# Performance work log

Measured on AMD Instinct MI355X. Metric: run time of the kernel, lower is better.

Reference implementation:

```python
import jax, jax.numpy as jnp
import numpy as np

N = 50000
E = 800000
D = 128
L = 3


def gru_cell(m, h, w_ih, w_hh, b_ih, b_hh):
    # m, h: [N, D]; w_ih, w_hh: [3D, D]; b_ih, b_hh: [3D]
    gi = m @ w_ih.T + b_ih  # [N, 3D]
    gh = h @ w_hh.T + b_hh  # [N, 3D]
    i_r, i_z, i_n = jnp.split(gi, 3, axis=-1)
    h_r, h_z, h_n = jnp.split(gh, 3, axis=-1)
    r = jax.nn.sigmoid(i_r + h_r)
    z = jax.nn.sigmoid(i_z + h_z)
    n = jnp.tanh(i_n + r * h_n)
    return (1.0 - z) * n + z * h


def setup_inputs() -> dict:
    key = jax.random.key(0)
    ks = jax.random.split(key, 8)
    s = 1.0 / np.sqrt(D)
    z = jax.random.normal(ks[0], (N, D), dtype=jnp.float32)
    edge_index = jax.random.randint(ks[1], (2, E), 0, N, dtype=jnp.int64)
    weight = jax.random.uniform(ks[2], (L, D, D), dtype=jnp.float32, minval=-s, maxval=s)
    w_ih = jax.random.uniform(ks[3], (3 * D, D), dtype=jnp.float32, minval=-s, maxval=s)
    w_hh = jax.random.uniform(ks[4], (3 * D, D), dtype=jnp.float32, minval=-s, maxval=s)
    b_ih = jax.random.uniform(ks[5], (3 * D,), dtype=jnp.float32, minval=-s, maxval=s)
    b_hh = jax.random.uniform(ks[6], (3 * D,), dtype=jnp.float32, minval=-s, maxval=s)
    return {"z": z, "edge_index": edge_index, "weight": weight,
            "w_ih": w_ih, "w_hh": w_hh, "b_ih": b_ih, "b_hh": b_hh}


def reference(z, edge_index, weight, w_ih, w_hh, b_ih, b_hh):
    # GatedGraphConv: per layer, m = h @ W_l; aggregate m[src] into dst (sum); GRU update.
    src, dst = edge_index[0], edge_index[1]
    h = z  # in_channels == out_channels, no padding
    for l in range(L):
        m = h @ weight[l]                              # [N, D]
        agg = jax.ops.segment_sum(m[src], dst, num_segments=N)  # scatter-add over edges
        h = gru_cell(agg, h, w_ih, w_hh, b_ih, b_hh)
    return h
```

## Files before the change

### kernel.cpp

```cpp
#include <hip/hip_runtime.h>
#include <hip/hip_bf16.h>

#define NN 50000
#define NE 800000
#define D 128
#define NL 3
#define G3 384

typedef __attribute__((ext_vector_type(4))) float f32x4;
typedef __attribute__((ext_vector_type(2))) float f32x2;
typedef _Float16 f16;
typedef __attribute__((ext_vector_type(8))) _Float16 f16x8;
typedef __attribute__((ext_vector_type(2))) _Float16 f16x2;

__global__ void detect_i64_kernel(const int* __restrict__ ei, int* __restrict__ flag) {
    __shared__ int any_nz;
    if (threadIdx.x == 0) any_nz = 0;
    __syncthreads();
    int v = ei[threadIdx.x * 2 + 1];
    if (v != 0) atomicOr(&any_nz, 1);
    __syncthreads();
    if (threadIdx.x == 0) *flag = (any_nz == 0) ? 1 : 0;
}

static __device__ __forceinline__ void load_edge(const int* ei, const int* flag, int e,
                                                 int& src, int& dst) {
    if (*flag) {
        src = ei[2LL * e];
        dst = ei[2LL * (NE + e)];
    } else {
        src = ei[e];
        dst = ei[NE + e];
    }
}

__global__ void hist_kernel(const int* __restrict__ ei, const int* __restrict__ flag,
                            int* __restrict__ counts, unsigned short* __restrict__ rank16) {
    int e = blockIdx.x * blockDim.x + threadIdx.x;
    if (e >= NE) return;
    int src, dst;
    load_edge(ei, flag, e, src, dst);
    rank16[e] = (unsigned short)atomicAdd(counts + dst, 1);
}

#define SBLK 256
#define NSB ((NN + SBLK - 1) / SBLK)

__global__ __launch_bounds__(SBLK) void scan_reduce_kernel(const int* __restrict__ counts,
                                                           int* __restrict__ block_sums) {
    __shared__ int lds[SBLK];
    int i = blockIdx.x * SBLK + threadIdx.x;
    lds[threadIdx.x] = (i < NN) ? counts[i] : 0;
    __syncthreads();
    for (int off = SBLK / 2; off > 0; off >>= 1) {
        if (threadIdx.x < off) lds[threadIdx.x] += lds[threadIdx.x + off];
        __syncthreads();
    }
    if (threadIdx.x == 0) block_sums[blockIdx.x] = lds[0];
}

__global__ __launch_bounds__(256) void scan_offsets_kernel(const int* __restrict__ block_sums,
                                                           int* __restrict__ block_off,
                                                           int* __restrict__ row_start) {
    __shared__ int lds[256];
    int t = threadIdx.x;
    int v = (t < NSB) ? block_sums[t] : 0;
    lds[t] = v;
    __syncthreads();
    for (int off = 1; off < 256; off <<= 1) {
        int x = (t >= off) ? lds[t - off] : 0;
        __syncthreads();
        lds[t] += x;
        __syncthreads();
    }
    if (t < NSB) block_off[t] = lds[t] - v;
    if (t == 255) row_start[NN] = lds[255];
}

__global__ __launch_bounds__(SBLK) void scan_final_kernel(const int* __restrict__ counts,
                                                          const int* __restrict__ block_off,
                                                          int* __restrict__ row_start) {
    __shared__ int lds[SBLK];
    int i = blockIdx.x * SBLK + threadIdx.x;
    int v = (i < NN) ? counts[i] : 0;
    lds[threadIdx.x] = v;
    __syncthreads();
    for (int off = 1; off < SBLK; off <<= 1) {
        int x = (threadIdx.x >= off) ? lds[threadIdx.x - off] : 0;
        __syncthreads();
        lds[threadIdx.x] += x;
        __syncthreads();
    }
    if (i < NN) row_start[i] = block_off[blockIdx.x] + lds[threadIdx.x] - v;
}

__global__ void fill_kernel(const int* __restrict__ ei, const int* __restrict__ flag,
                            const int* __restrict__ row_start,
                            const unsigned short* __restrict__ rank16,
                            unsigned short* __restrict__ csr16) {
    int e = blockIdx.x * blockDim.x + threadIdx.x;
    if (e >= NE) return;
    int src, dst;
    load_edge(ei, flag, e, src, dst);
    csr16[row_start[dst] + (int)rank16[e]] = (unsigned short)src;
}

__global__ void init_h_kernel(const float* __restrict__ z, f16* __restrict__ h) {
    int i = blockIdx.x * blockDim.x + threadIdx.x;
    if (i * 2 >= NN * D) return;
    f32x2 v = *(const f32x2*)(z + i * 2);
    f16x2 o = {(f16)v[0], (f16)v[1]};
    *(f16x2*)(h + i * 2) = o;
}

__global__ __launch_bounds__(256) void gather_kernel(
    const f16* __restrict__ h, const int* __restrict__ row_start,
    const unsigned short* __restrict__ csr16, f16* __restrict__ agg) {
    int row = blockIdx.x * 4 + (threadIdx.x >> 6);
    if (row >= NN) return;
    int lane = threadIdx.x & 63;
    int eslot = lane >> 4;
    int c0 = (lane & 15) * 8;
    int beg = row_start[row], end = row_start[row + 1];
    float acc[8] = {0.f, 0.f, 0.f, 0.f, 0.f, 0.f, 0.f, 0.f};
    for (int base = beg; base + eslot < end; base += 4) {
        int s = (int)csr16[base + eslot];
        f16x8 v = *(const f16x8*)(h + s * D + c0);
#pragma unroll
        for (int j = 0; j < 8; ++j) acc[j] += (float)v[j];
    }
#pragma unroll
    for (int j = 0; j < 8; ++j) {
        acc[j] += __shfl_xor(acc[j], 16, 64);
        acc[j] += __shfl_xor(acc[j], 32, 64);
    }
    if (lane < 16) {
        f16x8 o;
#pragma unroll
        for (int j = 0; j < 8; ++j) o[j] = (f16)acc[j];
        *(f16x8*)(agg + row * D + c0) = o;
    }
}

__global__ void precompute_weights(const float* __restrict__ weight,
                                   const float* __restrict__ w_ih,
                                   const float* __restrict__ w_hh,
                                   f16* __restrict__ wct, f16* __restrict__ whh) {
    int l = blockIdx.x / G3;
    int g = blockIdx.x % G3;
    int c = threadIdx.x;
    __shared__ float wih_row[D];
    wih_row[c] = w_ih[g * D + c];
    __syncthreads();
    const float* wrow = weight + ((long long)l * D + c) * D;
    float acc = 0.f;
#pragma unroll 8
    for (int j = 0; j < D; ++j) acc += wrow[j] * wih_row[j];
    wct[((long long)l * G3 + g) * D + c] = (f16)acc;
    if (l == 0) whh[g * D + c] = (f16)w_hh[g * D + c];
}

#define TMG 128
#define MFMA_F16 __builtin_amdgcn_mfma_f32_16x16x32_f16
__global__ __launch_bounds__(512) void gru_fused_kernel(
    const f16* __restrict__ agg, const f16* __restrict__ hin, f16* __restrict__ hout,
    const f16* __restrict__ wct, const f16* __restrict__ whh,
    const float* __restrict__ b_ih, const float* __restrict__ b_hh, int ndt,
    float* __restrict__ out_f32) {
    __shared__ char wlds[6 * 4096];
    const int tid = threadIdx.x;
    const int lane = tid & 63;
    const int wv = tid >> 6;
    const int fr = lane & 15;
    const int kg = lane >> 4;
    const int m0 = blockIdx.x * TMG;
    const int dt0 = blockIdx.y * ndt;

    int arow = m0 + wv * 16 + fr;
    int arc = arow < NN ? arow : NN - 1;
    const int abase = arc * D;

    f16x8 fa[4], fh[4];
#pragma unroll
    for (int ks = 0; ks < 4; ++ks) {
        int k0 = ks * 32 + kg * 8;
        fa[ks] = *(const f16x8*)(agg + abase + k0);
        fh[ks] = *(const f16x8*)(hin + abase + k0);
    }

#pragma unroll 1
    for (int dti = 0; dti < ndt; ++dti) {
        const int dt = dt0 + dti;
        const int gr = dt * 16;
        if (dti) __syncthreads();
#pragma unroll
        for (int p3 = 0; p3 < 3; ++p3) {
            int unit = tid + p3 * 512;
            int panel = unit >> 8;
            int u = unit & 255;
            int sr = u >> 4;
            int sc = (u & 15) * 8;
            const f16* srcp = (panel < 3)
                                  ? wct + (panel * 128 + gr + sr) * D + sc
                                  : whh + ((panel - 3) * 128 + gr + sr) * D + sc;
            int wb = (u * 16) ^ ((sr & 7) << 4);
            *(f16x8*)(wlds + panel * 4096 + wb) = *(const f16x8*)srcp;
        }
        __syncthreads();

        f32x4 a_ir = {0, 0, 0, 0}, a_iz = {0, 0, 0, 0}, a_in = {0, 0, 0, 0};
        f32x4 a_hr = {0, 0, 0, 0}, a_hz = {0, 0, 0, 0}, a_hn = {0, 0, 0, 0};
#pragma unroll
        for (int ks = 0; ks < 4; ++ks) {
            const int kb = fr * 256 + (((ks * 4 + kg) ^ (fr & 7)) << 4);
            f16x8 bir = *(const f16x8*)(wlds + 0 * 4096 + kb);
            f16x8 biz = *(const f16x8*)(wlds + 1 * 4096 + kb);
            f16x8 bin = *(const f16x8*)(wlds + 2 * 4096 + kb);
            f16x8 bhr = *(const f16x8*)(wlds + 3 * 4096 + kb);
            f16x8 bhz = *(const f16x8*)(wlds + 4 * 4096 + kb);
            f16x8 bhn = *(const f16x8*)(wlds + 5 * 4096 + kb);
            a_ir = MFMA_F16(fa[ks], bir, a_ir, 0, 0, 0);
            a_iz = MFMA_F16(fa[ks], biz, a_iz, 0, 0, 0);
            a_in = MFMA_F16(fa[ks], bin, a_in, 0, 0, 0);
            a_hr = MFMA_F16(fh[ks], bhr, a_hr, 0, 0, 0);
            a_hz = MFMA_F16(fh[ks], bhz, a_hz, 0, 0, 0);
            a_hn = MFMA_F16(fh[ks], bhn, a_hn, 0, 0, 0);
        }
        const int d = gr + fr;
        float bir_ = b_ih[d], biz_ = b_ih[128 + d], bin_ = b_ih[256 + d];
        float bhr_ = b_hh[d], bhz_ = b_hh[128 + d], bhn_ = b_hh[256 + d];
#pragma unroll
        for (int j = 0; j < 4; ++j) {
            int row = m0 + wv * 16 + kg * 4 + j;
            if (row >= NN) continue;
            float ir = a_ir[j] + bir_, iz = a_iz[j] + biz_, in_ = a_in[j] + bin_;
            float hr = a_hr[j] + bhr_, hz = a_hz[j] + bhz_, hn = a_hn[j] + bhn_;
            float r = 1.f / (1.f + __expf(-(ir + hr)));
            float zz = 1.f / (1.f + __expf(-(iz + hz)));
            float e2 = __expf(2.f * (in_ + r * hn));
            float nn = 1.f - 2.f / (e2 + 1.f);
            int off = row * D + d;
            float hold = (float)hin[off];
            float hnew = (1.f - zz) * nn + zz * hold;
            if (out_f32)
                out_f32[off] = hnew;
            else
                hout[off] = (f16)hnew;
        }
    }
}

extern "C" void kernel_launch(void* const* d_in, const int* in_sizes, int n_in,
                              void* d_out, int out_size, void* d_ws, size_t ws_size,
                              hipStream_t stream) {
    const float* z = (const float*)d_in[0];
    const int* ei = (const int*)d_in[1];
    const float* weight = (const float*)d_in[2];
    const float* w_ih = (const float*)d_in[3];
    const float* w_hh = (const float*)d_in[4];
    const float* b_ih = (const float*)d_in[5];
    const float* b_hh = (const float*)d_in[6];
    float* out = (float*)d_out;

    char* ws = (char*)d_ws;
    size_t off = 0;
    f16* wct = (f16*)(ws + off); off += 294912;
    f16* whh = (f16*)(ws + off); off += 98304;
    int* flag       = (int*)(ws + off); off += 256;
    int* counts     = (int*)(ws + off); off += (size_t)NN * 4;
    int* row_start  = (int*)(ws + off); off += (size_t)(NN + 16) * 4;
    int* block_sums = (int*)(ws + off); off += (size_t)NSB * 4;
    int* block_off  = (int*)(ws + off); off += (size_t)NSB * 4;
    unsigned short* rank16 = (unsigned short*)(ws + off); off += (size_t)NE * 2;
    unsigned short* csr16  = (unsigned short*)(ws + off); off += (size_t)NE * 2;
    f16* agg  = (f16*)(ws + off); off += (size_t)NN * D * 2;
    f16* hA   = (f16*)(ws + off); off += (size_t)NN * D * 2;
    size_t off_min = off;
    f16* hB   = (f16*)(ws + off); off += (size_t)NN * D * 2;
    const bool split = (ws_size >= off);
    if (!split) { hB = hA; (void)off_min; }

    detect_i64_kernel<<<1, 256, 0, stream>>>(ei, flag);
    hipMemsetAsync(counts, 0, (size_t)NN * 4, stream);
    hist_kernel<<<(NE + 255) / 256, 256, 0, stream>>>(ei, flag, counts, rank16);
    scan_reduce_kernel<<<NSB, SBLK, 0, stream>>>(counts, block_sums);
    scan_offsets_kernel<<<1, 256, 0, stream>>>(block_sums, block_off, row_start);
    scan_final_kernel<<<NSB, SBLK, 0, stream>>>(counts, block_off, row_start);
    fill_kernel<<<(NE + 255) / 256, 256, 0, stream>>>(ei, flag, row_start, rank16, csr16);
    precompute_weights<<<NL * G3, 128, 0, stream>>>(weight, w_ih, w_hh, wct, whh);
    const int npair = NN * D / 2;
    init_h_kernel<<<(npair + 255) / 256, 256, 0, stream>>>(z, hA);

    const int ndt = split ? 2 : 8;
    const dim3 gg((NN + TMG - 1) / TMG, split ? 4 : 1);
    const f16* cin = hA;
    for (int l = 0; l < NL; ++l) {
        gather_kernel<<<(NN + 3) / 4, 256, 0, stream>>>(cin, row_start, csr16, agg);
        f16* cout = split ? ((cin == hA) ? hB : hA) : (f16*)cin;
        long long woff = (long long)l * G3 * D;
        float* last_out = (l == NL - 1) ? out : nullptr;
        gru_fused_kernel<<<gg, 512, 0, stream>>>(agg, cin, cout, wct + woff, whh,
                                                 b_ih, b_hh, ndt, last_out);
        cin = cout;
    }
}
```

Before: 309.4 us.

## Unroll gather with dual accumulators and stage all GRU weight tiles at once

The gather loop now processes two edge batches per iteration into two accumulators, so more independent row loads are in flight. The fused GRU kernel fixes NDT at 2 and loads both column tiles' weight panels into a larger shared buffer in one pass with a single barrier, instead of reloading and syncing per tile. A separate fallback kernel that reads weights directly from global memory handles the case where the workspace is too small for double-buffered h. The change doubles the GRU kernel's shared-memory footprint, which may lower occupancy.

```diff
diff --git a/kernel.cpp b/kernel.cpp
--- a/kernel.cpp
+++ b/kernel.cpp
@@ -123,14 +123,25 @@
     int c0 = (lane & 15) * 8;
     int beg = row_start[row], end = row_start[row + 1];
     float acc[8] = {0.f, 0.f, 0.f, 0.f, 0.f, 0.f, 0.f, 0.f};
-    for (int base = beg; base + eslot < end; base += 4) {
-        int s = (int)csr16[base + eslot];
+    float acc2[8] = {0.f, 0.f, 0.f, 0.f, 0.f, 0.f, 0.f, 0.f};
+    int e = beg;
+    for (; e + 7 < end; e += 8) {
+        int s0 = (int)csr16[e + eslot];
+        int s1 = (int)csr16[e + eslot + 4];
+        f16x8 v0 = *(const f16x8*)(h + s0 * D + c0);
+        f16x8 v1 = *(const f16x8*)(h + s1 * D + c0);
+#pragma unroll
+        for (int j = 0; j < 8; ++j) { acc[j] += (float)v0[j]; acc2[j] += (float)v1[j]; }
+    }
+    for (; e + eslot < end; e += 4) {
+        int s = (int)csr16[e + eslot];
         f16x8 v = *(const f16x8*)(h + s * D + c0);
 #pragma unroll
         for (int j = 0; j < 8; ++j) acc[j] += (float)v[j];
     }
 #pragma unroll
     for (int j = 0; j < 8; ++j) {
+        acc[j] += acc2[j];
         acc[j] += __shfl_xor(acc[j], 16, 64);
         acc[j] += __shfl_xor(acc[j], 32, 64);
     }
@@ -161,20 +172,21 @@
 }
 
 #define TMG 128
+#define NDT 2
 #define MFMA_F16 __builtin_amdgcn_mfma_f32_16x16x32_f16
 __global__ __launch_bounds__(512) void gru_fused_kernel(
     const f16* __restrict__ agg, const f16* __restrict__ hin, f16* __restrict__ hout,
     const f16* __restrict__ wct, const f16* __restrict__ whh,
-    const float* __restrict__ b_ih, const float* __restrict__ b_hh, int ndt,
+    const float* __restrict__ b_ih, const float* __restrict__ b_hh,
     float* __restrict__ out_f32) {
-    __shared__ char wlds[6 * 4096];
+    __shared__ char wlds[NDT * 6 * 4096];
     const int tid = threadIdx.x;
     const int lane = tid & 63;
     const int wv = tid >> 6;
     const int fr = lane & 15;
     const int kg = lane >> 4;
     const int m0 = blockIdx.x * TMG;
-    const int dt0 = blockIdx.y * ndt;
+    const int dt0 = blockIdx.y * NDT;
 
     int arow = m0 + wv * 16 + fr;
     int arc = arow < NN ? arow : NN - 1;
@@ -188,37 +200,39 @@
         fh[ks] = *(const f16x8*)(hin + abase + k0);
     }
 
-#pragma unroll 1
-    for (int dti = 0; dti < ndt; ++dti) {
-        const int dt = dt0 + dti;
-        const int gr = dt * 16;
-        if (dti) __syncthreads();
-#pragma unroll
-        for (int p3 = 0; p3 < 3; ++p3) {
-            int unit = tid + p3 * 512;
-            int panel = unit >> 8;
-            int u = unit & 255;
-            int sr = u >> 4;
-            int sc = (u & 15) * 8;
-            const f16* srcp = (panel < 3)
-                                  ? wct + (panel * 128 + gr + sr) * D + sc
-                                  : whh + ((panel - 3) * 128 + gr + sr) * D + sc;
-            int wb = (u * 16) ^ ((sr & 7) << 4);
-            *(f16x8*)(wlds + panel * 4096 + wb) = *(const f16x8*)srcp;
-        }
-        __syncthreads();
-
+#pragma unroll
+    for (int p6 = 0; p6 < NDT * 3; ++p6) {
+        int unit = tid + p6 * 512;
+        int dpanel = unit >> 8;
+        int dti = dpanel / 6;
+        int panel = dpanel % 6;
+        int u = unit & 255;
+        int sr = u >> 4;
+        int sc = (u & 15) * 8;
+        int gr = (dt0 + dti) * 16;
+        const f16* srcp = (panel < 3)
+                              ? wct + (panel * 128 + gr + sr) * D + sc
+                              : whh + ((panel - 3) * 128 + gr + sr) * D + sc;
+        int wb = (u * 16) ^ ((sr & 7) << 4);
+        *(f16x8*)(wlds + dpanel * 4096 + wb) = *(const f16x8*)srcp;
+    }
+    __syncthreads();
+
+#pragma unroll
+    for (int dti = 0; dti < NDT; ++dti) {
+        const int gr = (dt0 + dti) * 16;
+        const char* wb0 = wlds + dti * 6 * 4096;
         f32x4 a_ir = {0, 0, 0, 0}, a_iz = {0, 0, 0, 0}, a_in = {0, 0, 0, 0};
         f32x4 a_hr = {0, 0, 0, 0}, a_hz = {0, 0, 0, 0}, a_hn = {0, 0, 0, 0};
 #pragma unroll
         for (int ks = 0; ks < 4; ++ks) {
             const int kb = fr * 256 + (((ks * 4 + kg) ^ (fr & 7)) << 4);
-            f16x8 bir = *(const f16x8*)(wlds + 0 * 4096 + kb);
-            f16x8 biz = *(const f16x8*)(wlds + 1 * 4096 + kb);
-            f16x8 bin = *(const f16x8*)(wlds + 2 * 4096 + kb);
-            f16x8 bhr = *(const f16x8*)(wlds + 3 * 4096 + kb);
-            f16x8 bhz = *(const f16x8*)(wlds + 4 * 4096 + kb);
-            f16x8 bhn = *(const f16x8*)(wlds + 5 * 4096 + kb);
+            f16x8 bir = *(const f16x8*)(wb0 + 0 * 4096 + kb);
+            f16x8 biz = *(const f16x8*)(wb0 + 1 * 4096 + kb);
+            f16x8 bin = *(const f16x8*)(wb0 + 2 * 4096 + kb);
+            f16x8 bhr = *(const f16x8*)(wb0 + 3 * 4096 + kb);
+            f16x8 bhz = *(const f16x8*)(wb0 + 4 * 4096 + kb);
+            f16x8 bhn = *(const f16x8*)(wb0 + 5 * 4096 + kb);
             a_ir = MFMA_F16(fa[ks], bir, a_ir, 0, 0, 0);
             a_iz = MFMA_F16(fa[ks], biz, a_iz, 0, 0, 0);
             a_in = MFMA_F16(fa[ks], bin, a_in, 0, 0, 0);
@@ -250,6 +264,72 @@
     }
 }
 
+__global__ __launch_bounds__(256) void gru_fused_fallback(
+    const f16* __restrict__ agg, const f16* __restrict__ hin, f16* __restrict__ hout,
+    const f16* __restrict__ wct, const f16* __restrict__ whh,
+    const float* __restrict__ b_ih, const float* __restrict__ b_hh,
+    float* __restrict__ out_f32) {
+    const int tid = threadIdx.x;
+    const int lane = tid & 63;
+    const int wv = tid >> 6;
+    const int fr = lane & 15;
+    const int kg = lane >> 4;
+    const int m0 = blockIdx.x * 64;
+    int arow = m0 + wv * 16 + fr;
+    int arc = arow < NN ? arow : NN - 1;
+    const int abase = arc * D;
+    f16x8 fa[4], fh[4];
+#pragma unroll
+    for (int ks = 0; ks < 4; ++ks) {
+        int k0 = ks * 32 + kg * 8;
+        fa[ks] = *(const f16x8*)(agg + abase + k0);
+        fh[ks] = *(const f16x8*)(hin + abase + k0);
+    }
+#pragma unroll 1
+    for (int dt = 0; dt < 8; ++dt) {
+        const int g = dt * 16 + fr;
+        f32x4 a_ir = {0, 0, 0, 0}, a_iz = {0, 0, 0, 0}, a_in = {0, 0, 0, 0};
+        f32x4 a_hr = {0, 0, 0, 0}, a_hz = {0, 0, 0, 0}, a_hn = {0, 0, 0, 0};
+#pragma unroll
+        for (int ks = 0; ks < 4; ++ks) {
+            int k0 = ks * 32 + kg * 8;
+            f16x8 bir = *(const f16x8*)(wct + (g)*D + k0);
+            f16x8 biz = *(const f16x8*)(wct + (128 + g) * D + k0);
+            f16x8 bin = *(const f16x8*)(wct + (256 + g) * D + k0);
+            f16x8 bhr = *(const f16x8*)(whh + (g)*D + k0);
+            f16x8 bhz = *(const f16x8*)(whh + (128 + g) * D + k0);
+            f16x8 bhn = *(const f16x8*)(whh + (256 + g) * D + k0);
+            a_ir = MFMA_F16(fa[ks], bir, a_ir, 0, 0, 0);
+            a_iz = MFMA_F16(fa[ks], biz, a_iz, 0, 0, 0);
+            a_in = MFMA_F16(fa[ks], bin, a_in, 0, 0, 0);
+            a_hr = MFMA_F16(fh[ks], bhr, a_hr, 0, 0, 0);
+            a_hz = MFMA_F16(fh[ks], bhz, a_hz, 0, 0, 0);
+            a_hn = MFMA_F16(fh[ks], bhn, a_hn, 0, 0, 0);
+        }
+        const int d = g;
+        float bir_ = b_ih[d], biz_ = b_ih[128 + d], bin_ = b_ih[256 + d];
+        float bhr_ = b_hh[d], bhz_ = b_hh[128 + d], bhn_ = b_hh[256 + d];
+#pragma unroll
+        for (int j = 0; j < 4; ++j) {
+            int row = m0 + wv * 16 + kg * 4 + j;
+            if (row >= NN) continue;
+            float ir = a_ir[j] + bir_, iz = a_iz[j] + biz_, in_ = a_in[j] + bin_;
+            float hr = a_hr[j] + bhr_, hz = a_hz[j] + bhz_, hn = a_hn[j] + bhn_;
+            float r = 1.f / (1.f + __expf(-(ir + hr)));
+            float zz = 1.f / (1.f + __expf(-(iz + hz)));
+            float e2 = __expf(2.f * (in_ + r * hn));
+            float nn = 1.f - 2.f / (e2 + 1.f);
+            int off = row * D + d;
+            float hold = (float)hin[off];
+            float hnew = (1.f - zz) * nn + zz * hold;
+            if (out_f32)
+                out_f32[off] = hnew;
+            else
+                hout[off] = (f16)hnew;
+        }
+    }
+}
+
 extern "C" void kernel_launch(void* const* d_in, const int* in_sizes, int n_in,
                               void* d_out, int out_size, void* d_ws, size_t ws_size,
                               hipStream_t stream) {
@@ -275,10 +355,9 @@
     unsigned short* csr16  = (unsigned short*)(ws + off); off += (size_t)NE * 2;
     f16* agg  = (f16*)(ws + off); off += (size_t)NN * D * 2;
     f16* hA   = (f16*)(ws + off); off += (size_t)NN * D * 2;
-    size_t off_min = off;
     f16* hB   = (f16*)(ws + off); off += (size_t)NN * D * 2;
     const bool split = (ws_size >= off);
-    if (!split) { hB = hA; (void)off_min; }
+    if (!split) hB = hA;
 
     detect_i64_kernel<<<1, 256, 0, stream>>>(ei, flag);
     hipMemsetAsync(counts, 0, (size_t)NN * 4, stream);
@@ -291,16 +370,20 @@
     const int npair = NN * D / 2;
     init_h_kernel<<<(npair + 255) / 256, 256, 0, stream>>>(z, hA);
 
-    const int ndt = split ? 2 : 8;
-    const dim3 gg((NN + TMG - 1) / TMG, split ? 4 : 1);
+    const dim3 gg((NN + TMG - 1) / TMG, 8 / NDT);
     const f16* cin = hA;
     for (int l = 0; l < NL; ++l) {
         gather_kernel<<<(NN + 3) / 4, 256, 0, stream>>>(cin, row_start, csr16, agg);
         f16* cout = split ? ((cin == hA) ? hB : hA) : (f16*)cin;
         long long woff = (long long)l * G3 * D;
         float* last_out = (l == NL - 1) ? out : nullptr;
-        gru_fused_kernel<<<gg, 512, 0, stream>>>(agg, cin, cout, wct + woff, whh,
-                                                 b_ih, b_hh, ndt, last_out);
+        if (split) {
+            gru_fused_kernel<<<gg, 512, 0, stream>>>(agg, cin, cout, wct + woff, whh,
+                                                     b_ih, b_hh, last_out);
+        } else {
+            gru_fused_fallback<<<(NN + 63) / 64, 256, 0, stream>>>(
+                agg, cin, cout, wct + woff, whh, b_ih, b_hh, last_out);
+        }
         cin = cout;
     }
 }
```

Measured after the change: 297.6 us. 1.04x faster.
